# Kernel tuning notes

Hardware: AMD Instinct MI355X
Metric: run time of the kernel (lower is better)

## Reference

```python
import jax, jax.numpy as jnp
import numpy as np

EPS = 1e-5


def bin_act(x):
    # forward of Binaryactivation: sign (STE backward handled in fwdbwd module)
    return jnp.sign(x)


def bin_conv(x, w, stride, padding):
    # per-output-filter scaling factor = mean |w| over (in, kh, kw), detached
    scale = jax.lax.stop_gradient(jnp.mean(jnp.abs(w), axis=(1, 2, 3), keepdims=True))
    bw = scale * jnp.sign(w)
    rw = jnp.clip(w, -1.0, 1.0)
    # STE blend: forward uses binary weight, backward flows through clamp(w)
    filt = jax.lax.stop_gradient(bw - rw) + rw
    return jax.lax.conv_general_dilated(
        x, filt, window_strides=(stride, stride),
        padding=[(padding, padding), (padding, padding)],
        dimension_numbers=("NCHW", "OIHW", "NCHW"))


def batchnorm(x, gamma, beta):
    # training-mode BN: biased batch stats over (N, H, W)
    mean = jnp.mean(x, axis=(0, 2, 3), keepdims=True)
    var = jnp.mean((x - mean) ** 2, axis=(0, 2, 3), keepdims=True)
    xn = (x - mean) * jax.lax.rsqrt(var + EPS)
    return xn * gamma[None, :, None, None] + beta[None, :, None, None]


def prelu(x, a):
    a = a[None, :, None, None]
    return jnp.where(x >= 0, x, a * x)


def addbias(x, b):
    return x + b[None, :, None, None]


def setup_inputs() -> dict:
    key = jax.random.key(0)
    ks = jax.random.split(key, 4)
    C = 256
    x = jax.random.normal(ks[0], (32, C, 56, 56), dtype=jnp.float32)
    # BinaryConv weights init: uniform[0, 0.001)
    w3x3 = jax.random.uniform(ks[1], (C, C, 3, 3), dtype=jnp.float32) * 0.001
    wres = jax.random.uniform(ks[2], (C, C, 1, 1), dtype=jnp.float32) * 0.001
    zeros = jnp.zeros((C,), dtype=jnp.float32)
    ones = jnp.ones((C,), dtype=jnp.float32)
    prelu_init = jnp.full((C,), 0.25, dtype=jnp.float32)
    return {
        "x": x,
        "b1_1": zeros, "w3x3": w3x3, "bn1_g": ones, "bn1_b": zeros,
        "b1_2": zeros, "prelu1_a": prelu_init, "b1_3": zeros,
        "b2_1": zeros, "wres": wres, "bn2_g": ones, "bn2_b": zeros,
        "b2_2": zeros, "prelu2_a": prelu_init, "b2_3": zeros,
    }


def reference(x, b1_1, w3x3, bn1_g, bn1_b, b1_2, prelu1_a, b1_3,
              b2_1, wres, bn2_g, bn2_b, b2_2, prelu2_a, b2_3):
    # branch 1: bias -> sign -> binary 3x3 conv -> BN -> residual add
    x1 = bin_act(addbias(x, b1_1))
    x1 = bin_conv(x1, w3x3, stride=1, padding=1)
    x1 = batchnorm(x1, bn1_g, bn1_b)
    x = x + x1
    x = addbias(x, b1_2)
    x = prelu(x, prelu1_a)
    x = addbias(x, b1_3)
    # branch 2 (in_channel == out_channel): binary 1x1 conv residual
    x2 = bin_act(addbias(x, b2_1))
    x2 = bin_conv(x2, wres, stride=1, padding=0)
    x2 = batchnorm(x2, bn2_g, bn2_b)
    x2 = x2 + x
    x2 = addbias(x2, b2_2)
    x2 = prelu(x2, prelu2_a)
    x2 = addbias(x2, b2_3)
    return x2
```

## Files before the change

kernel.cpp:

```cpp
#include <hip/hip_runtime.h>
#include <cstdint>
#include <math.h>

#define HW    3136
#define NPIX  100352
#define NELEM 25690112

#define OFF_PW1   0u
#define OFF_PW2   73728u
#define OFF_CORR  81920u
#define OFF_SC1   86016u
#define OFF_SC2   87040u
#define OFF_A1    88064u
#define OFF_B1    89088u
#define OFF_A2    90112u
#define OFF_B2    91136u
#define OFF_ST    92160u
#define ST_BYTES  524288u
#define OFF_P1    616448u
#define OFF_P2    3827712u
#define OFF_S1    7038976u
#define OFF_S2    58419200u

__global__ void prep_w_k(const float* __restrict__ w3, const float* __restrict__ wr,
                         uint32_t* __restrict__ pw1, uint32_t* __restrict__ pw2,
                         float* __restrict__ sc1, float* __restrict__ sc2,
                         short* __restrict__ corrG) {
  const int o = blockIdx.x, l = threadIdx.x;
  const float* wo = w3 + (size_t)o * 2304;
  float s = 0.f;
  for (int i = l; i < 2304; i += 64) s += fabsf(wo[i]);
  for (int m = 32; m; m >>= 1) s += __shfl_xor(s, m, 64);
  if (l == 0) sc1[o] = s / 2304.0f;
  int wsum[9];
  for (int tap = 0; tap < 9; ++tap) {
    int cnt = 0;
    for (int jp = 0; jp < 4; ++jp) {
      float wv = wo[(size_t)(jp * 64 + l) * 9 + tap];
      unsigned long long m = __ballot(wv >= 0.0f);
      cnt += __popcll(m);
      if (l == 0) {
        pw1[(size_t)(o * 9 + tap) * 8 + jp * 2 + 0] = (uint32_t)m;
        pw1[(size_t)(o * 9 + tap) * 8 + jp * 2 + 1] = (uint32_t)(m >> 32);
      }
    }
    wsum[tap] = 2 * cnt - 256;
  }
  if (l == 0) {
    corrG[o * 8 + 0] = (short)(wsum[0] + wsum[1] + wsum[2]);
    corrG[o * 8 + 1] = (short)(wsum[6] + wsum[7] + wsum[8]);
    corrG[o * 8 + 2] = (short)(wsum[0] + wsum[3] + wsum[6]);
    corrG[o * 8 + 3] = (short)(wsum[2] + wsum[5] + wsum[8]);
    corrG[o * 8 + 4] = (short)wsum[0];
    corrG[o * 8 + 5] = (short)wsum[2];
    corrG[o * 8 + 6] = (short)wsum[6];
    corrG[o * 8 + 7] = (short)wsum[8];
  }
  const float* wro = wr + (size_t)o * 256;
  float s2 = 0.f;
  for (int i = l; i < 256; i += 64) s2 += fabsf(wro[i]);
  for (int m = 32; m; m >>= 1) s2 += __shfl_xor(s2, m, 64);
  if (l == 0) sc2[o] = s2 / 256.0f;
  for (int jp = 0; jp < 4; ++jp) {
    unsigned long long m = __ballot(wro[jp * 64 + l] >= 0.0f);
    if (l == 0) {
      pw2[(size_t)o * 8 + jp * 2 + 0] = (uint32_t)m;
      pw2[(size_t)o * 8 + jp * 2 + 1] = (uint32_t)(m >> 32);
    }
  }
}

__global__ __launch_bounds__(256) void pack1_k(const float* __restrict__ x,
                                               const float* __restrict__ b1_1,
                                               uint32_t* __restrict__ p1) {
  const int j = blockIdx.y;
  const int gpx = blockIdx.x * 256 + threadIdx.x;
  const int n = gpx / 784;
  const int p4 = (gpx - n * 784) * 4;
  const float* xb = x + ((size_t)n * 256 + j * 32) * HW + p4;
  uint32_t w0 = 0, w1 = 0, w2 = 0, w3 = 0;
#pragma unroll
  for (int cc = 0; cc < 32; ++cc) {
    float4 v = *(const float4*)(xb + (size_t)cc * HW);
    float bb = b1_1[j * 32 + cc];
    w0 |= (v.x + bb >= 0.f) ? (1u << cc) : 0u;
    w1 |= (v.y + bb >= 0.f) ? (1u << cc) : 0u;
    w2 |= (v.z + bb >= 0.f) ? (1u << cc) : 0u;
    w3 |= (v.w + bb >= 0.f) ? (1u << cc) : 0u;
  }
  uint4 o = {w0, w1, w2, w3};
  *(uint4*)&p1[(size_t)j * NPIX + gpx * 4] = o;
}

__global__ __launch_bounds__(256, 3) void conv1_k(const uint32_t* __restrict__ p1,
    const uint32_t* __restrict__ pw1, const short* __restrict__ corrG,
    short* __restrict__ S1, unsigned long long* __restrict__ st1) {
  __shared__ uint32_t actS[1680];
  __shared__ uint32_t wtS[9216];
  __shared__ short    corrS[1024];
  const int tid = threadIdx.x;
  const int bx = blockIdx.x;
  const int ty = bx / 7, tx = bx % 7;
  const int by = blockIdx.y;
  const int zh = blockIdx.z;
  const int h0 = ty * 8 - 1, w0 = tx * 8 - 1;
  for (int i = tid; i < 1600; i += 256) {
    int img = i / 800, rem = i % 800;
    int r = rem / 80, c = (rem % 80) / 8, q = i & 7;
    int hh = h0 + r, ww = w0 + c;
    uint32_t v = 0;
    if ((unsigned)hh < 56u && (unsigned)ww < 56u)
      v = p1[q * NPIX + (by * 2 + img) * HW + hh * 56 + ww];
    actS[img * 840 + r * 84 + c * 8 + q] = v;
  }
  for (int i = tid; i < 2304; i += 256)
    ((uint4*)wtS)[i] = ((const uint4*)(pw1 + (size_t)zh * 9216))[i];
  if (tid < 128)
    ((uint4*)corrS)[tid] = ((const uint4*)(corrG + zh * 1024))[tid];
  __syncthreads();

  const int chg = tid & 7;
  const int pr = (tid >> 3) & 7;
  const int wave = tid >> 6;
  const int img = wave >> 1;
  const int chalf = wave & 1;
  const int cb = chalf * 8 + chg;
  const uint32_t* actB = actS + img * 840;

  int acc[8][8];
#pragma unroll
  for (int j = 0; j < 8; ++j)
#pragma unroll
    for (int k = 0; k < 8; ++k) acc[j][k] = 0;

#pragma unroll 1
  for (int dh = 0; dh < 3; ++dh) {
#pragma unroll 1
    for (int q4 = 0; q4 < 2; ++q4) {
      uint4 a10[10];
      const uint32_t* ar = actB + (pr + dh) * 84 + q4 * 4;
#pragma unroll
      for (int c2 = 0; c2 < 10; ++c2) a10[c2] = *(const uint4*)(ar + c2 * 8);
#pragma unroll
      for (int dw = 0; dw < 3; ++dw) {
        const uint32_t* wr_ = wtS + cb * 72 + (dh * 3 + dw) * 8 + q4 * 4;
#pragma unroll
        for (int j = 0; j < 8; ++j) {
          uint4 w = *(const uint4*)(wr_ + j * 1152);
#pragma unroll
          for (int k = 0; k < 8; ++k) {
            uint4 a = a10[k + dw];
            acc[j][k] += __builtin_popcount(a.x ^ w.x) + __builtin_popcount(a.y ^ w.y)
                       + __builtin_popcount(a.z ^ w.z) + __builtin_popcount(a.w ^ w.w);
          }
        }
      }
    }
  }

  const int n = by * 2 + img;
  const int h = ty * 8 + pr;
  const bool hT = (h == 0), hB = (h == 55);
  const int slot = (bx + by * 49 + zh * 784) & 63;
#pragma unroll
  for (int j = 0; j < 8; ++j) {
    const int ch_l = cb + 16 * j;
    const short* cw = &corrS[ch_l * 8];
    int cH = hT ? (int)cw[0] : (hB ? (int)cw[1] : 0);
    int s[8];
#pragma unroll
    for (int k = 0; k < 8; ++k) s[k] = 2304 - 2 * acc[j][k] + cH;
    if (tx == 0) s[0] += (int)cw[2] - (hT ? (int)cw[4] : (hB ? (int)cw[6] : 0));
    if (tx == 6) s[7] += (int)cw[3] - (hT ? (int)cw[5] : (hB ? (int)cw[7] : 0));
    int sm = 0, sq = 0;
#pragma unroll
    for (int k = 0; k < 8; ++k) { sm += s[k]; sq += s[k] * s[k]; }
    uint4 val;
    val.x = (uint32_t)(uint16_t)s[0] | ((uint32_t)(uint16_t)s[1] << 16);
    val.y = (uint32_t)(uint16_t)s[2] | ((uint32_t)(uint16_t)s[3] << 16);
    val.z = (uint32_t)(uint16_t)s[4] | ((uint32_t)(uint16_t)s[5] << 16);
    val.w = (uint32_t)(uint16_t)s[6] | ((uint32_t)(uint16_t)s[7] << 16);
    *(uint4*)&S1[(((size_t)n * 49 + bx) * 256 + zh * 128 + ch_l) * 64 + pr * 8] = val;
#pragma unroll
    for (int m = 8; m < 64; m <<= 1) { sm += __shfl_xor(sm, m, 64); sq += __shfl_xor(sq, m, 64); }
    if (pr == 0) {
      unsigned long long* st = st1 + ((size_t)(zh * 128 + ch_l) * 64 + slot) * 2;
      atomicAdd(&st[0], (unsigned long long)(long long)sm);
      atomicAdd(&st[1], (unsigned long long)(long long)sq);
    }
  }
}

__global__ void bnfin_k(const unsigned long long* __restrict__ st, const float* __restrict__ sc,
                        const float* __restrict__ g, const float* __restrict__ b,
                        float* __restrict__ A, float* __restrict__ B) {
  const int c = blockIdx.x, l = threadIdx.x;
  long long sm = (long long)st[((size_t)c * 64 + l) * 2 + 0];
  long long sq = (long long)st[((size_t)c * 64 + l) * 2 + 1];
  for (int m = 1; m < 64; m <<= 1) { sm += __shfl_xor(sm, m, 64); sq += __shfl_xor(sq, m, 64); }
  if (l == 0) {
    const double M = (double)NPIX;
    double mS = (double)sm / M;
    double vS = (double)sq / M - mS * mS;
    double scale = (double)sc[c];
    double mean = scale * mS;
    double var = scale * scale * vS;
    double rstd = 1.0 / sqrt(var + 1e-5);
    double gd = (double)g[c];
    A[c] = (float)(gd * scale * rstd);
    B[c] = (float)((double)b[c] - gd * mean * rstd);
  }
}

__global__ __launch_bounds__(256) void pack2_k(const float* __restrict__ x,
    const short* __restrict__ S1,
    const float* __restrict__ A1, const float* __restrict__ B1,
    const float* __restrict__ b1_2, const float* __restrict__ a1,
    const float* __restrict__ b1_3, const float* __restrict__ b2_1,
    uint32_t* __restrict__ p2) {
  const int j = blockIdx.y;
  const int gpx = blockIdx.x * 256 + threadIdx.x;
  const int n = gpx / 784;
  const int p4 = (gpx - n * 784) * 4;
  const int h = p4 / 56, w = p4 - (p4 / 56) * 56;
  const int tile = (h >> 3) * 7 + (w >> 3);
  const int px = (h & 7) * 8 + (w & 7);
  const float* xb = x + ((size_t)n * 256 + j * 32) * HW + p4;
  const short* s1b = S1 + (((size_t)n * 49 + tile) * 256 + j * 32) * 64 + px;
  uint32_t w0 = 0, w1 = 0, w2 = 0, w3 = 0;
#pragma unroll
  for (int cc = 0; cc < 32; ++cc) {
    int c = j * 32 + cc;
    float4 xv = *(const float4*)(xb + (size_t)cc * HW);
    short4 s1 = *(const short4*)(s1b + cc * 64);
    float Ac = A1[c], Bc = B1[c], p12 = b1_2[c], al = a1[c], p13 = b1_3[c], p21 = b2_1[c];
    float u, v, t;
    u = xv.x + (Ac * (float)s1.x + Bc) + p12; v = u >= 0.f ? u : al * u; t = v + p13 + p21;
    w0 |= (t >= 0.f) ? (1u << cc) : 0u;
    u = xv.y + (Ac * (float)s1.y + Bc) + p12; v = u >= 0.f ? u : al * u; t = v + p13 + p21;
    w1 |= (t >= 0.f) ? (1u << cc) : 0u;
    u = xv.z + (Ac * (float)s1.z + Bc) + p12; v = u >= 0.f ? u : al * u; t = v + p13 + p21;
    w2 |= (t >= 0.f) ? (1u << cc) : 0u;
    u = xv.w + (Ac * (float)s1.w + Bc) + p12; v = u >= 0.f ? u : al * u; t = v + p13 + p21;
    w3 |= (t >= 0.f) ? (1u << cc) : 0u;
  }
  uint4 o = {w0, w1, w2, w3};
  *(uint4*)&p2[(size_t)j * NPIX + gpx * 4] = o;
}

__global__ __launch_bounds__(256) void conv2_k(const uint32_t* __restrict__ p2,
                                               const uint32_t* __restrict__ pw2,
                                               short* __restrict__ S2,
                                               unsigned long long* __restrict__ st2) {
  __shared__ uint32_t actS[512];
  __shared__ uint32_t wtS[1024];
  const int tid = threadIdx.x;
  const int bx = blockIdx.x;
  const int zh = blockIdx.y;
  const int pg0 = bx * 64;
  for (int i = tid; i < 512; i += 256) {
    int gq = i >> 2, ws_ = i & 3;
    int pxl = gq >> 1, q4 = gq & 1;
    int q = q4 * 4 + ws_;
    actS[((gq ^ ((gq >> 3) & 15)) << 2) + ws_] = p2[q * NPIX + pg0 + pxl];
  }
  if (tid < 256)
    ((uint4*)wtS)[tid] = ((const uint4*)(pw2 + zh * 1024))[tid];
  __syncthreads();
  const int pxg = tid & 15, chg = tid >> 4;
  int acc[8][4];
#pragma unroll
  for (int j = 0; j < 8; ++j)
#pragma unroll
    for (int k = 0; k < 4; ++k) acc[j][k] = 0;
#pragma unroll
  for (int q4 = 0; q4 < 2; ++q4) {
    uint4 a[4];
#pragma unroll
    for (int k = 0; k < 4; ++k) {
      int gq = 8 * pxg + 2 * k + q4;
      a[k] = *(const uint4*)&actS[(gq ^ pxg) << 2];
    }
#pragma unroll
    for (int j = 0; j < 8; ++j) {
      uint4 w = *(const uint4*)&wtS[(chg + 16 * j) * 8 + q4 * 4];
#pragma unroll
      for (int k = 0; k < 4; ++k)
        acc[j][k] += __builtin_popcount(a[k].x ^ w.x) + __builtin_popcount(a[k].y ^ w.y)
                   + __builtin_popcount(a[k].z ^ w.z) + __builtin_popcount(a[k].w ^ w.w);
    }
  }
  const int slot = bx & 63;
#pragma unroll
  for (int j = 0; j < 8; ++j) {
    const int c_l = chg + 16 * j;
    int s[4], sm = 0, sq = 0;
#pragma unroll
    for (int k = 0; k < 4; ++k) {
      s[k] = 256 - 2 * acc[j][k];
      sm += s[k]; sq += s[k] * s[k];
    }
    short4 o4;
    o4.x = (short)s[0]; o4.y = (short)s[1]; o4.z = (short)s[2]; o4.w = (short)s[3];
    *(short4*)&S2[(((size_t)bx * 256) + zh * 128 + c_l) * 64 + pxg * 4] = o4;
#pragma unroll
    for (int m = 1; m < 16; m <<= 1) { sm += __shfl_xor(sm, m, 64); sq += __shfl_xor(sq, m, 64); }
    if (pxg == 0) {
      unsigned long long* st = st2 + ((size_t)(zh * 128 + c_l) * 64 + slot) * 2;
      atomicAdd(&st[0], (unsigned long long)(long long)sm);
      atomicAdd(&st[1], (unsigned long long)(long long)sq);
    }
  }
}

__global__ __launch_bounds__(256) void final_k(const float* __restrict__ x,
    const short* __restrict__ S1, const short* __restrict__ S2,
    const float* __restrict__ A1, const float* __restrict__ B1,
    const float* __restrict__ b1_2, const float* __restrict__ a1, const float* __restrict__ b1_3,
    const float* __restrict__ A2, const float* __restrict__ B2,
    const float* __restrict__ b2_2, const float* __restrict__ a2, const float* __restrict__ b2_3,
    float* __restrict__ out) {
  const int gi = blockIdx.x * 256 + threadIdx.x;
  const int i4 = gi * 4;
  const int nc = i4 / 3136;
  const int p = i4 - nc * 3136;
  const int n = nc >> 8, c = nc & 255;
  const int h = p / 56, w = p - (p / 56) * 56;
  const int tile = (h >> 3) * 7 + (w >> 3);
  const int px = (h & 7) * 8 + (w & 7);
  short4 s1 = *(const short4*)&S1[(((size_t)n * 49 + tile) * 256 + c) * 64 + px];
  const int pg = n * 3136 + p;
  short4 s2 = *(const short4*)&S2[((size_t)(pg >> 6) * 256 + c) * 64 + (pg & 63)];
  float4 xv = *(const float4*)&x[i4];
  const float A1c = A1[c], B1c = B1[c], P12 = b1_2[c], AL1 = a1[c], P13 = b1_3[c];
  const float A2c = A2[c], B2c = B2[c], P22 = b2_2[c], AL2 = a2[c], P23 = b2_3[c];
  float xs[4] = {xv.x, xv.y, xv.z, xv.w};
  float f1[4] = {(float)s1.x, (float)s1.y, (float)s1.z, (float)s1.w};
  float f2[4] = {(float)s2.x, (float)s2.y, (float)s2.z, (float)s2.w};
  float o[4];
#pragma unroll
  for (int e = 0; e < 4; ++e) {
    float u = xs[e] + (A1c * f1[e] + B1c);
    u = u + P12;
    float v = u >= 0.0f ? u : AL1 * u;
    float t = v + P13;
    float z = (A2c * f2[e] + B2c) + t;
    z = z + P22;
    float vv = z >= 0.0f ? z : AL2 * z;
    o[e] = vv + P23;
  }
  float4 ov = {o[0], o[1], o[2], o[3]};
  *(float4*)&out[i4] = ov;
}

extern "C" void kernel_launch(void* const* d_in, const int* in_sizes, int n_in,
                              void* d_out, int out_size, void* d_ws, size_t ws_size,
                              hipStream_t stream) {
  const float* x    = (const float*)d_in[0];
  const float* b1_1 = (const float*)d_in[1];
  const float* w3x3 = (const float*)d_in[2];
  const float* bn1g = (const float*)d_in[3];
  const float* bn1b = (const float*)d_in[4];
  const float* b1_2 = (const float*)d_in[5];
  const float* a1   = (const float*)d_in[6];
  const float* b1_3 = (const float*)d_in[7];
  const float* b2_1 = (const float*)d_in[8];
  const float* wres = (const float*)d_in[9];
  const float* bn2g = (const float*)d_in[10];
  const float* bn2b = (const float*)d_in[11];
  const float* b2_2 = (const float*)d_in[12];
  const float* a2   = (const float*)d_in[13];
  const float* b2_3 = (const float*)d_in[14];

  char* ws = (char*)d_ws;
  uint32_t* pw1 = (uint32_t*)(ws + OFF_PW1);
  uint32_t* pw2 = (uint32_t*)(ws + OFF_PW2);
  short* corrG = (short*)(ws + OFF_CORR);
  float* sc1 = (float*)(ws + OFF_SC1);
  float* sc2 = (float*)(ws + OFF_SC2);
  float* A1 = (float*)(ws + OFF_A1);
  float* B1 = (float*)(ws + OFF_B1);
  float* A2 = (float*)(ws + OFF_A2);
  float* B2 = (float*)(ws + OFF_B2);
  unsigned long long* st1 = (unsigned long long*)(ws + OFF_ST);
  unsigned long long* st2 = (unsigned long long*)(ws + OFF_ST + 262144u);
  uint32_t* p1 = (uint32_t*)(ws + OFF_P1);
  uint32_t* p2 = (uint32_t*)(ws + OFF_P2);
  short* S1 = (short*)(ws + OFF_S1);
  short* S2 = (short*)(ws + OFF_S2);

  hipMemsetAsync(ws + OFF_ST, 0, ST_BYTES, stream);
  prep_w_k<<<256, 64, 0, stream>>>(w3x3, wres, pw1, pw2, sc1, sc2, corrG);
  pack1_k<<<dim3(98, 8), 256, 0, stream>>>(x, b1_1, p1);
  conv1_k<<<dim3(49, 16, 2), 256, 0, stream>>>(p1, pw1, corrG, S1, st1);
  bnfin_k<<<256, 64, 0, stream>>>(st1, sc1, bn1g, bn1b, A1, B1);
  pack2_k<<<dim3(98, 8), 256, 0, stream>>>(x, S1, A1, B1, b1_2, a1, b1_3, b2_1, p2);
  conv2_k<<<dim3(1568, 2), 256, 0, stream>>>(p2, pw2, S2, st2);
  bnfin_k<<<256, 64, 0, stream>>>(st2, sc2, bn2g, bn2b, A2, B2);
  final_k<<<25088, 256, 0, stream>>>(x, S1, S2, A1, B1, b1_2, a1, b1_3,
                                     A2, B2, b2_2, a2, b2_3, (float*)d_out);
}
```

Baseline: 508.5 us.

## Retile binary 3x3 conv to one image per block with padded weight layout

conv1 now handles one image per block instead of two, so the grid doubles in y. Each thread holds 4 output channels by 8 pixels instead of 8 by 8, and the whole block shares one activation tile. Weight rows in shared memory are padded from 72 to 76 words to avoid LDS bank conflicts, and the popcount sums are split into serial adds on the accumulator. This cuts register pressure (the occupancy hint of 3 is dropped) and raises parallelism, but weights are reloaded per image and more global atomics are issued.

```diff
diff --git a/kernel.cpp b/kernel.cpp
--- a/kernel.cpp
+++ b/kernel.cpp
@@ -92,44 +92,43 @@
   *(uint4*)&p1[(size_t)j * NPIX + gpx * 4] = o;
 }
 
-__global__ __launch_bounds__(256, 3) void conv1_k(const uint32_t* __restrict__ p1,
+__global__ __launch_bounds__(256) void conv1_k(const uint32_t* __restrict__ p1,
     const uint32_t* __restrict__ pw1, const short* __restrict__ corrG,
     short* __restrict__ S1, unsigned long long* __restrict__ st1) {
-  __shared__ uint32_t actS[1680];
-  __shared__ uint32_t wtS[9216];
+  __shared__ uint32_t actS[840];
+  __shared__ uint32_t wtS[9728];
   __shared__ short    corrS[1024];
   const int tid = threadIdx.x;
   const int bx = blockIdx.x;
   const int ty = bx / 7, tx = bx % 7;
-  const int by = blockIdx.y;
+  const int n = blockIdx.y;
   const int zh = blockIdx.z;
   const int h0 = ty * 8 - 1, w0 = tx * 8 - 1;
-  for (int i = tid; i < 1600; i += 256) {
-    int img = i / 800, rem = i % 800;
-    int r = rem / 80, c = (rem % 80) / 8, q = i & 7;
+  for (int i = tid; i < 800; i += 256) {
+    int r = i / 80, cq = i % 80;
+    int c = cq >> 3;
     int hh = h0 + r, ww = w0 + c;
     uint32_t v = 0;
     if ((unsigned)hh < 56u && (unsigned)ww < 56u)
-      v = p1[q * NPIX + (by * 2 + img) * HW + hh * 56 + ww];
-    actS[img * 840 + r * 84 + c * 8 + q] = v;
-  }
-  for (int i = tid; i < 2304; i += 256)
-    ((uint4*)wtS)[i] = ((const uint4*)(pw1 + (size_t)zh * 9216))[i];
+      v = p1[(size_t)(cq & 7) * NPIX + (size_t)n * HW + hh * 56 + ww];
+    actS[r * 84 + cq] = v;
+  }
+  const uint32_t* pwB = pw1 + (size_t)zh * 9216;
+  for (int i = tid; i < 2304; i += 256) {
+    int ch = i / 18, t4 = (i % 18) * 4;
+    *(uint4*)&wtS[ch * 76 + t4] = *(const uint4*)(pwB + ch * 72 + t4);
+  }
   if (tid < 128)
     ((uint4*)corrS)[tid] = ((const uint4*)(corrG + zh * 1024))[tid];
   __syncthreads();
 
-  const int chg = tid & 7;
-  const int pr = (tid >> 3) & 7;
-  const int wave = tid >> 6;
-  const int img = wave >> 1;
-  const int chalf = wave & 1;
-  const int cb = chalf * 8 + chg;
-  const uint32_t* actB = actS + img * 840;
-
-  int acc[8][8];
-#pragma unroll
-  for (int j = 0; j < 8; ++j)
+  const int pr = tid & 7;
+  const int chg = tid >> 3;
+  const uint32_t* wp = wtS + chg * 76;
+
+  int acc[4][8];
+#pragma unroll
+  for (int j = 0; j < 4; ++j)
 #pragma unroll
     for (int k = 0; k < 8; ++k) acc[j][k] = 0;
 
@@ -138,33 +137,35 @@
 #pragma unroll 1
     for (int q4 = 0; q4 < 2; ++q4) {
       uint4 a10[10];
-      const uint32_t* ar = actB + (pr + dh) * 84 + q4 * 4;
+      const uint32_t* ar = actS + (pr + dh) * 84 + q4 * 4;
 #pragma unroll
       for (int c2 = 0; c2 < 10; ++c2) a10[c2] = *(const uint4*)(ar + c2 * 8);
 #pragma unroll
       for (int dw = 0; dw < 3; ++dw) {
-        const uint32_t* wr_ = wtS + cb * 72 + (dh * 3 + dw) * 8 + q4 * 4;
-#pragma unroll
-        for (int j = 0; j < 8; ++j) {
-          uint4 w = *(const uint4*)(wr_ + j * 1152);
+#pragma unroll
+        for (int j = 0; j < 4; ++j) {
+          uint4 w = *(const uint4*)(wp + j * 2432 + (dh * 3 + dw) * 8 + q4 * 4);
 #pragma unroll
           for (int k = 0; k < 8; ++k) {
             uint4 a = a10[k + dw];
-            acc[j][k] += __builtin_popcount(a.x ^ w.x) + __builtin_popcount(a.y ^ w.y)
-                       + __builtin_popcount(a.z ^ w.z) + __builtin_popcount(a.w ^ w.w);
+            int t = acc[j][k];
+            t += __builtin_popcount(a.x ^ w.x);
+            t += __builtin_popcount(a.y ^ w.y);
+            t += __builtin_popcount(a.z ^ w.z);
+            t += __builtin_popcount(a.w ^ w.w);
+            acc[j][k] = t;
           }
         }
       }
     }
   }
 
-  const int n = by * 2 + img;
   const int h = ty * 8 + pr;
   const bool hT = (h == 0), hB = (h == 55);
-  const int slot = (bx + by * 49 + zh * 784) & 63;
-#pragma unroll
-  for (int j = 0; j < 8; ++j) {
-    const int ch_l = cb + 16 * j;
+  const int slot = (bx + n * 49) & 63;
+#pragma unroll
+  for (int j = 0; j < 4; ++j) {
+    const int ch_l = chg + 32 * j;
     const short* cw = &corrS[ch_l * 8];
     int cH = hT ? (int)cw[0] : (hB ? (int)cw[1] : 0);
     int s[8];
@@ -182,7 +183,7 @@
     val.w = (uint32_t)(uint16_t)s[6] | ((uint32_t)(uint16_t)s[7] << 16);
     *(uint4*)&S1[(((size_t)n * 49 + bx) * 256 + zh * 128 + ch_l) * 64 + pr * 8] = val;
 #pragma unroll
-    for (int m = 8; m < 64; m <<= 1) { sm += __shfl_xor(sm, m, 64); sq += __shfl_xor(sq, m, 64); }
+    for (int m = 1; m < 8; m <<= 1) { sm += __shfl_xor(sm, m, 64); sq += __shfl_xor(sq, m, 64); }
     if (pr == 0) {
       unsigned long long* st = st1 + ((size_t)(zh * 128 + ch_l) * 64 + slot) * 2;
       atomicAdd(&st[0], (unsigned long long)(long long)sm);
@@ -285,9 +286,14 @@
     for (int j = 0; j < 8; ++j) {
       uint4 w = *(const uint4*)&wtS[(chg + 16 * j) * 8 + q4 * 4];
 #pragma unroll
-      for (int k = 0; k < 4; ++k)
-        acc[j][k] += __builtin_popcount(a[k].x ^ w.x) + __builtin_popcount(a[k].y ^ w.y)
-                   + __builtin_popcount(a[k].z ^ w.z) + __builtin_popcount(a[k].w ^ w.w);
+      for (int k = 0; k < 4; ++k) {
+        int t = acc[j][k];
+        t += __builtin_popcount(a[k].x ^ w.x);
+        t += __builtin_popcount(a[k].y ^ w.y);
+        t += __builtin_popcount(a[k].z ^ w.z);
+        t += __builtin_popcount(a[k].w ^ w.w);
+        acc[j][k] = t;
+      }
     }
   }
   const int slot = bx & 63;
@@ -392,7 +398,7 @@
   hipMemsetAsync(ws + OFF_ST, 0, ST_BYTES, stream);
   prep_w_k<<<256, 64, 0, stream>>>(w3x3, wres, pw1, pw2, sc1, sc2, corrG);
   pack1_k<<<dim3(98, 8), 256, 0, stream>>>(x, b1_1, p1);
-  conv1_k<<<dim3(49, 16, 2), 256, 0, stream>>>(p1, pw1, corrG, S1, st1);
+  conv1_k<<<dim3(49, 32, 2), 256, 0, stream>>>(p1, pw1, corrG, S1, st1);
   bnfin_k<<<256, 64, 0, stream>>>(st1, sc1, bn1g, bn1b, A1, B1);
   pack2_k<<<dim3(98, 8), 256, 0, stream>>>(x, S1, A1, B1, b1_2, a1, b1_3, b2_1, p2);
   conv2_k<<<dim3(1568, 2), 256, 0, stream>>>(p2, pw2, S2, st2);
```

Result: no change. 500.8 us (-1.5%).
